# Performance work log

Measured on AMD Instinct MI355X. Metric: run time of the kernel, lower is better.

The kernel has to match this reference:

```python
import jax, jax.numpy as jnp
import numpy as np


def setup_inputs() -> dict:
    key = jax.random.key(0)
    gramBatch = jax.random.normal(key, (8, 8, 1024, 16, 16), dtype=jnp.float32)
    return {"gramBatch": gramBatch, "patchPerRow": 32}


def reference(gramBatch, patchPerRow):
    # Parallel (parralelMode=True) path of GramDistMap.forward.
    B, C, N, D1, D2 = gramBatch.shape
    g = gramBatch.reshape(B, C, N, D1 * D2)            # [B,C,N,D]
    # gramNorm = sqrt(sum((g*g)^2)) = sqrt(sum(g^4))
    g2 = g * g
    norm = jnp.sqrt(jnp.sum(g2 * g2, axis=-1))         # [B,C,N]
    # sum_d (g_i - g_j)^2 = ||g_i||^2 + ||g_j||^2 - 2 g_i . g_j,
    # computed without materializing the [B,C,N,N,D] broadcast tensor.
    sq = jnp.sum(g2, axis=-1)                          # [B,C,N]
    dots = jnp.einsum('bcnd,bcmd->bcnm', g, g)         # [B,C,N,N]
    dist2 = sq[..., :, None] + sq[..., None, :] - 2.0 * dots
    distMat = dist2 / (norm[..., :, None] * norm[..., None, :])
    return distMat.mean(axis=1)                        # [B,N,N]
```

## Files before the change

kernel.cpp:

```cpp
#include <hip/hip_runtime.h>
#include <stdint.h>

#define NB 8
#define NC 8
#define NN 1024
#define ND 256
#define KK 2048
#define BM 128
#define BN 64
#define BKK 64
#define NT (KK / BKK)

typedef float f32x4 __attribute__((ext_vector_type(4)));
typedef short bf16x8 __attribute__((ext_vector_type(8)));

__device__ __forceinline__ unsigned short f2bf(float x) {
  union { float f; uint32_t u; } a; a.f = x;
  uint32_t u = a.u;
  return (unsigned short)((u + 0x7FFFu + ((u >> 16) & 1u)) >> 16);
}

__device__ __forceinline__ void gload16(const void* g, void* l) {
  __builtin_amdgcn_global_load_lds(
      (__attribute__((address_space(1))) uint32_t*)g,
      (__attribute__((address_space(3))) uint32_t*)l, 16, 0, 0);
}

__global__ __launch_bounds__(256) void prep_kernel(
    const float* __restrict__ g, unsigned short* __restrict__ ghat,
    float* __restrict__ uFlat, float* __restrict__ vFlat) {
  int wid = blockIdx.x * 4 + (threadIdx.x >> 6);
  int lane = threadIdx.x & 63;
#pragma unroll
  for (int j = 0; j < 4; ++j) {
    int rowid = wid * 4 + j;
    int n = rowid & (NN - 1);
    int bc = rowid >> 10;
    int c = bc & (NC - 1);
    int b = bc >> 3;
    const float* row = g + (size_t)rowid * ND;
    f32x4 v = *(const f32x4*)(row + lane * 4);
    float s2 = 0.f, s4 = 0.f;
#pragma unroll
    for (int q = 0; q < 4; ++q) { float x2 = v[q] * v[q]; s2 += x2; s4 += x2 * x2; }
#pragma unroll
    for (int off = 32; off; off >>= 1) {
      s2 += __shfl_xor(s2, off);
      s4 += __shfl_xor(s4, off);
    }
    float rn = rsqrtf(s4);
    ushort4 o;
    o.x = f2bf(v[0] * rn); o.y = f2bf(v[1] * rn);
    o.z = f2bf(v[2] * rn); o.w = f2bf(v[3] * rn);
    size_t gh = ((size_t)(b * NN + n)) * KK + (size_t)c * ND + lane * 4;
    *(ushort4*)(ghat + gh) = o;
    if (lane == 0) {
      uFlat[rowid] = s2 * rn;
      vFlat[rowid] = rn;
    }
  }
}

__global__ __launch_bounds__(256) void gram_gemm_kernel(
    const unsigned short* __restrict__ ghat,
    const float* __restrict__ uFlat, const float* __restrict__ vFlat,
    float* __restrict__ out) {
  __shared__ union {
    struct { unsigned short A[BM * BKK]; unsigned short Bt[BN * BKK]; } s;
    struct { float R[128][16]; float Cc[64][16]; } e;
  } sm;

  int bid = blockIdx.x;
  int logical = (bid & 7) * 128 + (bid >> 3);
  int b = logical >> 7;
  int t7 = logical & 127;
  int row0 = (t7 >> 4) * BM;
  int col0 = (t7 & 15) * BN;
  int tid = threadIdx.x;
  int lane = tid & 63;
  int wave = tid >> 6;
  int wr = (wave >> 1) * 64;
  int wc = (wave & 1) * 32;

  const unsigned short* gA = ghat + (size_t)(b * NN + row0) * KK;
  const unsigned short* gB = ghat + (size_t)(b * NN + col0) * KK;

  f32x4 acc[4][2];
#pragma unroll
  for (int i = 0; i < 4; ++i)
#pragma unroll
    for (int j = 0; j < 2; ++j)
      acc[i][j] = f32x4{0.f, 0.f, 0.f, 0.f};

  int rsel = lane & 15;
  int khalf = lane >> 4;
  int r8 = tid >> 3;
  int s8 = tid & 7;

  for (int t = 0; t < NT; ++t) {
    int k0 = t * BKK;
#pragma unroll
    for (int i = 0; i < 4; ++i) {
      int rr = i * 32 + r8;
      int sg = s8 ^ (rr & 7);
      gload16(gA + (size_t)rr * KK + k0 + sg * 8, sm.s.A + rr * BKK + s8 * 8);
    }
#pragma unroll
    for (int i = 0; i < 2; ++i) {
      int rr = i * 32 + r8;
      int sg = s8 ^ (rr & 7);
      gload16(gB + (size_t)rr * KK + k0 + sg * 8, sm.s.Bt + rr * BKK + s8 * 8);
    }
    __syncthreads();
#pragma unroll
    for (int kk = 0; kk < 2; ++kk) {
      bf16x8 af[4], bfb[2];
#pragma unroll
      for (int i = 0; i < 4; ++i) {
        int rr = wr + i * 16 + rsel;
        int slot = (kk * 4 + khalf) ^ (rr & 7);
        af[i] = *(const bf16x8*)&sm.s.A[rr * BKK + slot * 8];
      }
#pragma unroll
      for (int j = 0; j < 2; ++j) {
        int rr = wc + j * 16 + rsel;
        int slot = (kk * 4 + khalf) ^ (rr & 7);
        bfb[j] = *(const bf16x8*)&sm.s.Bt[rr * BKK + slot * 8];
      }
#pragma unroll
      for (int i = 0; i < 4; ++i)
#pragma unroll
        for (int j = 0; j < 2; ++j)
          acc[i][j] = __builtin_amdgcn_mfma_f32_16x16x32_bf16(af[i], bfb[j], acc[i][j], 0, 0, 0);
    }
    __syncthreads();
  }

  {
    int rl = tid >> 1;
    int half = tid & 1;
    const float* src = half ? vFlat : uFlat;
#pragma unroll
    for (int c = 0; c < 8; ++c)
      sm.e.R[rl][half * 8 + c] = src[(size_t)(b * NC + c) * NN + row0 + rl];
    if (rl < 64) {
#pragma unroll
      for (int c = 0; c < 8; ++c)
        sm.e.Cc[rl][half * 8 + c] = src[(size_t)(b * NC + c) * NN + col0 + rl];
    }
  }
  __syncthreads();

  int lr = (lane >> 4) * 4;
  int lc = lane & 15;
#pragma unroll
  for (int j = 0; j < 2; ++j) {
    int cl = wc + j * 16 + lc;
    f32x4 uc0 = *(const f32x4*)&sm.e.Cc[cl][0];
    f32x4 uc1 = *(const f32x4*)&sm.e.Cc[cl][4];
    f32x4 vc0 = *(const f32x4*)&sm.e.Cc[cl][8];
    f32x4 vc1 = *(const f32x4*)&sm.e.Cc[cl][12];
#pragma unroll
    for (int i = 0; i < 4; ++i) {
#pragma unroll
      for (int q = 0; q < 4; ++q) {
        int rl = wr + i * 16 + lr + q;
        f32x4 r0 = *(const f32x4*)&sm.e.R[rl][0];
        f32x4 r1 = *(const f32x4*)&sm.e.R[rl][4];
        f32x4 r2 = *(const f32x4*)&sm.e.R[rl][8];
        f32x4 r3 = *(const f32x4*)&sm.e.R[rl][12];
        float fr = r0[0]*vc0[0]+r0[1]*vc0[1]+r0[2]*vc0[2]+r0[3]*vc0[3]
                 + r1[0]*vc1[0]+r1[1]*vc1[1]+r1[2]*vc1[2]+r1[3]*vc1[3]
                 + r2[0]*uc0[0]+r2[1]*uc0[1]+r2[2]*uc0[2]+r2[3]*uc0[3]
                 + r3[0]*uc1[0]+r3[1]*uc1[1]+r3[2]*uc1[2]+r3[3]*uc1[3];
        float val = 0.125f * fr - 0.25f * acc[i][j][q];
        out[((size_t)(b * NN + row0 + rl)) * NN + (size_t)(col0 + cl)] = val;
      }
    }
  }
}

extern "C" void kernel_launch(void* const* d_in, const int* in_sizes, int n_in,
                              void* d_out, int out_size, void* d_ws, size_t ws_size,
                              hipStream_t stream) {
  const float* g = (const float*)d_in[0];
  unsigned short* ghat = (unsigned short*)d_ws;
  float* uFlat = (float*)((char*)d_ws + (size_t)NB * NN * KK * 2);
  float* vFlat = uFlat + (size_t)NB * NC * NN;
  float* outp = (float*)d_out;

  prep_kernel<<<NB * NC * NN / 16, 256, 0, stream>>>(g, ghat, uFlat, vFlat);
  gram_gemm_kernel<<<NB * 128 * 8 / 8 , 256, 0, stream>>>(ghat, uFlat, vFlat, outp);
}
```

Baseline: 210.9 us.

## Triple-buffer GEMM LDS tiles with async prefetch and restructure prep loads

The GEMM main loop now uses three LDS buffers, prefetching two K-tiles ahead with global_load_lds. It waits on vmcnt so only one barrier per iteration is needed, and raises wave priority around the MFMA section. This is meant to overlap global-to-LDS transfers with matrix math instead of stalling on a load, barrier, compute, barrier sequence. The prep kernel now assigns one 16-lane group per row with four vector loads per lane and a shorter shuffle reduction. LDS use triples to about 72 KB per block, which may reduce occupancy.

```diff
diff --git a/kernel.cpp b/kernel.cpp
--- a/kernel.cpp
+++ b/kernel.cpp
@@ -29,36 +29,38 @@
 __global__ __launch_bounds__(256) void prep_kernel(
     const float* __restrict__ g, unsigned short* __restrict__ ghat,
     float* __restrict__ uFlat, float* __restrict__ vFlat) {
-  int wid = blockIdx.x * 4 + (threadIdx.x >> 6);
-  int lane = threadIdx.x & 63;
-#pragma unroll
-  for (int j = 0; j < 4; ++j) {
-    int rowid = wid * 4 + j;
-    int n = rowid & (NN - 1);
-    int bc = rowid >> 10;
-    int c = bc & (NC - 1);
-    int b = bc >> 3;
-    const float* row = g + (size_t)rowid * ND;
-    f32x4 v = *(const f32x4*)(row + lane * 4);
-    float s2 = 0.f, s4 = 0.f;
-#pragma unroll
-    for (int q = 0; q < 4; ++q) { float x2 = v[q] * v[q]; s2 += x2; s4 += x2 * x2; }
-#pragma unroll
-    for (int off = 32; off; off >>= 1) {
-      s2 += __shfl_xor(s2, off);
-      s4 += __shfl_xor(s4, off);
-    }
-    float rn = rsqrtf(s4);
+  int tid = threadIdx.x;
+  int wave = tid >> 6, lane = tid & 63;
+  int sub = lane & 15, grp = lane >> 4;
+  int rowid = (blockIdx.x * 4 + wave) * 4 + grp;
+  const float* row = g + (size_t)rowid * ND;
+  f32x4 v[4];
+  float s2 = 0.f, s4 = 0.f;
+#pragma unroll
+  for (int q = 0; q < 4; ++q) {
+    v[q] = *(const f32x4*)(row + q * 64 + sub * 4);
+#pragma unroll
+    for (int e = 0; e < 4; ++e) { float x2 = v[q][e] * v[q][e]; s2 += x2; s4 += x2 * x2; }
+  }
+#pragma unroll
+  for (int off = 8; off; off >>= 1) {
+    s2 += __shfl_xor(s2, off);
+    s4 += __shfl_xor(s4, off);
+  }
+  float rn = rsqrtf(s4);
+  int n = rowid & (NN - 1);
+  int bc = rowid >> 10;
+  int c = bc & (NC - 1);
+  int b = bc >> 3;
+  unsigned short* dst = ghat + ((size_t)(b * NN + n)) * KK + (size_t)c * ND + sub * 4;
+#pragma unroll
+  for (int q = 0; q < 4; ++q) {
     ushort4 o;
-    o.x = f2bf(v[0] * rn); o.y = f2bf(v[1] * rn);
-    o.z = f2bf(v[2] * rn); o.w = f2bf(v[3] * rn);
-    size_t gh = ((size_t)(b * NN + n)) * KK + (size_t)c * ND + lane * 4;
-    *(ushort4*)(ghat + gh) = o;
-    if (lane == 0) {
-      uFlat[rowid] = s2 * rn;
-      vFlat[rowid] = rn;
-    }
-  }
+    o.x = f2bf(v[q][0] * rn); o.y = f2bf(v[q][1] * rn);
+    o.z = f2bf(v[q][2] * rn); o.w = f2bf(v[q][3] * rn);
+    *(ushort4*)(dst + q * 64) = o;
+  }
+  if (sub == 0) { uFlat[rowid] = s2 * rn; vFlat[rowid] = rn; }
 }
 
 __global__ __launch_bounds__(256) void gram_gemm_kernel(
@@ -66,7 +68,7 @@
     const float* __restrict__ uFlat, const float* __restrict__ vFlat,
     float* __restrict__ out) {
   __shared__ union {
-    struct { unsigned short A[BM * BKK]; unsigned short Bt[BN * BKK]; } s;
+    struct { unsigned short A[3][BM * BKK]; unsigned short Bt[3][BN * BKK]; } s;
     struct { float R[128][16]; float Cc[64][16]; } e;
   } sm;
 
@@ -97,21 +99,42 @@
   int r8 = tid >> 3;
   int s8 = tid & 7;
 
-  for (int t = 0; t < NT; ++t) {
+  auto STAGE = [&](int t, int bi) {
     int k0 = t * BKK;
 #pragma unroll
     for (int i = 0; i < 4; ++i) {
       int rr = i * 32 + r8;
       int sg = s8 ^ (rr & 7);
-      gload16(gA + (size_t)rr * KK + k0 + sg * 8, sm.s.A + rr * BKK + s8 * 8);
+      gload16(gA + (size_t)rr * KK + k0 + sg * 8, &sm.s.A[bi][rr * BKK + s8 * 8]);
     }
 #pragma unroll
     for (int i = 0; i < 2; ++i) {
       int rr = i * 32 + r8;
       int sg = s8 ^ (rr & 7);
-      gload16(gB + (size_t)rr * KK + k0 + sg * 8, sm.s.Bt + rr * BKK + s8 * 8);
-    }
-    __syncthreads();
+      gload16(gB + (size_t)rr * KK + k0 + sg * 8, &sm.s.Bt[bi][rr * BKK + s8 * 8]);
+    }
+  };
+
+  STAGE(0, 0);
+  STAGE(1, 1);
+
+  int cidx = 0;
+  for (int t = 0; t < NT; ++t) {
+    if (t + 1 < NT) {
+      asm volatile("s_waitcnt vmcnt(6)" ::: "memory");
+    } else {
+      asm volatile("s_waitcnt vmcnt(0)" ::: "memory");
+    }
+    __builtin_amdgcn_sched_barrier(0);
+    __builtin_amdgcn_s_barrier();
+    __builtin_amdgcn_sched_barrier(0);
+
+    if (t + 2 < NT) {
+      int pidx = cidx ? cidx - 1 : 2;
+      STAGE(t + 2, pidx);
+    }
+
+    __builtin_amdgcn_s_setprio(1);
 #pragma unroll
     for (int kk = 0; kk < 2; ++kk) {
       bf16x8 af[4], bfb[2];
@@ -119,13 +142,13 @@
       for (int i = 0; i < 4; ++i) {
         int rr = wr + i * 16 + rsel;
         int slot = (kk * 4 + khalf) ^ (rr & 7);
-        af[i] = *(const bf16x8*)&sm.s.A[rr * BKK + slot * 8];
+        af[i] = *(const bf16x8*)&sm.s.A[cidx][rr * BKK + slot * 8];
       }
 #pragma unroll
       for (int j = 0; j < 2; ++j) {
         int rr = wc + j * 16 + rsel;
         int slot = (kk * 4 + khalf) ^ (rr & 7);
-        bfb[j] = *(const bf16x8*)&sm.s.Bt[rr * BKK + slot * 8];
+        bfb[j] = *(const bf16x8*)&sm.s.Bt[cidx][rr * BKK + slot * 8];
       }
 #pragma unroll
       for (int i = 0; i < 4; ++i)
@@ -133,8 +156,11 @@
         for (int j = 0; j < 2; ++j)
           acc[i][j] = __builtin_amdgcn_mfma_f32_16x16x32_bf16(af[i], bfb[j], acc[i][j], 0, 0, 0);
     }
-    __syncthreads();
-  }
+    __builtin_amdgcn_s_setprio(0);
+
+    cidx = (cidx == 2) ? 0 : cidx + 1;
+  }
+  __syncthreads();
 
   {
     int rl = tid >> 1;
@@ -190,5 +216,5 @@
   float* outp = (float*)d_out;
 
   prep_kernel<<<NB * NC * NN / 16, 256, 0, stream>>>(g, ghat, uFlat, vFlat);
-  gram_gemm_kernel<<<NB * 128 * 8 / 8 , 256, 0, stream>>>(ghat, uFlat, vFlat, outp);
-}
+  gram_gemm_kernel<<<1024, 256, 0, stream>>>(ghat, uFlat, vFlat, outp);
+}
```

Result: slower. 216.5 us (+2.7%).
